# Kernel tuning notes

Measured on AMD Instinct MI355X. Metric: run time of the kernel, lower is better.

Reference implementation:

```python
import jax, jax.numpy as jnp
import numpy as np

N_NODES = 100000
NNZ = 3200000
D_FEAT = 128


def setup_inputs() -> dict:
    key = jax.random.key(0)
    k1, k2, k3 = jax.random.split(key, 3)
    indices = jax.random.randint(k1, (2, NNZ), 0, N_NODES, dtype=jnp.int64 if jax.config.jax_enable_x64 else jnp.int32)
    values = jax.random.normal(k2, (NNZ,), dtype=jnp.float32)
    b = jax.random.normal(k3, (N_NODES, D_FEAT), dtype=jnp.float32)
    return {"indices": indices, "values": values, "n_rows": N_NODES, "b": b}


def reference(indices, values, n_rows, b):
    # out = sparse_coo(indices, values, [n_rows, n_rows]) @ b
    # out[i] = sum_{e: row[e]==i} values[e] * b[col[e]]
    row, col = indices[0], indices[1]
    gathered = values[:, None] * b[col]              # [nnz, d]
    out = jax.ops.segment_sum(gathered, row, num_segments=n_rows)  # [n_rows, d]
    return out
```

## Files before the change

kernel.cpp:

```cpp
#include <hip/hip_runtime.h>


#define D_FEAT 128
#define RPB 256
#define BKT_SHIFT 8
#define MAX_NB 512
#define NBLK_SCAT 512
#define CHUNK_MAX 6400
#define STG_CAP 12288
#define RP_FLAG (1 << 30)

__device__ __forceinline__ unsigned short f2bf(float f) {
    unsigned u = __float_as_uint(f);
    u += 0x7FFFu + ((u >> 16) & 1u);
    return (unsigned short)(u >> 16);
}
__global__ void bconv_kernel(const float* __restrict__ bmat,
                             ushort* __restrict__ b16, int n4) {
    int i = blockIdx.x * blockDim.x + threadIdx.x;
    int gs = gridDim.x * blockDim.x;
    for (int k = i; k < n4; k += gs) {
        float4 v = reinterpret_cast<const float4*>(bmat)[k];
        ushort4 o;
        o.x = f2bf(v.x); o.y = f2bf(v.y); o.z = f2bf(v.z); o.w = f2bf(v.w);
        reinterpret_cast<ushort4*>(b16)[k] = o;
    }
}

__global__ void hist_kernel(const int* __restrict__ rowidx, int* __restrict__ hist,
                            int nnz) {
    __shared__ int lcnt[MAX_NB];
    for (int i = threadIdx.x; i < MAX_NB; i += blockDim.x) lcnt[i] = 0;
    __syncthreads();
    int gid = blockIdx.x * blockDim.x + threadIdx.x;
    int gsz = gridDim.x * blockDim.x;
    for (int e = gid; e < nnz; e += gsz)
        atomicAdd(&lcnt[rowidx[e] >> BKT_SHIFT], 1);
    __syncthreads();
    for (int i = threadIdx.x; i < MAX_NB; i += blockDim.x)
        if (lcnt[i]) atomicAdd(&hist[i], lcnt[i]);
}

__global__ void scan_kernel(const int* __restrict__ hist, int* __restrict__ gbase,
                            int* __restrict__ gcursor, int nb) {
    __shared__ int hs[512];
    int t = threadIdx.x;
    int v = hist[t];
    hs[t] = v;
    __syncthreads();
    for (int off = 1; off < 512; off <<= 1) {
        int u = (t >= off) ? hs[t - off] : 0;
        __syncthreads();
        hs[t] += u;
        __syncthreads();
    }
    int excl = hs[t] - v;
    if (t < nb) { gbase[t] = excl; gcursor[t] = excl; }
}

__global__ __launch_bounds__(512)
void scatter_kernel(const int* __restrict__ rowidx, const int* __restrict__ colidx,
                    const float* __restrict__ vals, int* __restrict__ gcursor,
                    float2* __restrict__ cv, int nnz, int nb) {
    __shared__ int loff[MAX_NB];
    __shared__ int cur[MAX_NB];
    __shared__ int gpos[MAX_NB];
    __shared__ ushort bktof[CHUNK_MAX];
    __shared__ float2 stage[CHUNK_MAX];
    int* scanbuf = (int*)stage;

    int t = threadIdx.x;
    int chunk = (nnz + gridDim.x - 1) / gridDim.x;
    int beg = blockIdx.x * chunk;
    int end = min(beg + chunk, nnz);
    int n = end - beg;

    for (int i = t; i < MAX_NB; i += 512) loff[i] = 0;
    __syncthreads();
    for (int e = beg + t; e < end; e += 512)
        atomicAdd(&loff[rowidx[e] >> BKT_SHIFT], 1);
    __syncthreads();

    int v = loff[t];
    scanbuf[t] = v;
    __syncthreads();
    for (int off = 1; off < 512; off <<= 1) {
        int u = (t >= off) ? scanbuf[t - off] : 0;
        __syncthreads();
        scanbuf[t] += u;
        __syncthreads();
    }
    int excl = scanbuf[t] - v;
    __syncthreads();
    loff[t] = excl;
    cur[t] = excl;
    __syncthreads();

    for (int e = beg + t; e < end; e += 512) {
        int r = rowidx[e];
        int bkt = r >> BKT_SHIFT;
        int pos = atomicAdd(&cur[bkt], 1);
        int pack = ((r & (RPB - 1)) << 17) | colidx[e];
        stage[pos] = make_float2(__int_as_float(pack), vals[e]);
        bktof[pos] = (ushort)bkt;
    }
    __syncthreads();

    if (t < nb) {
        int cnt = cur[t] - loff[t];
        if (cnt > 0) gpos[t] = atomicAdd(&gcursor[t], cnt);
    }
    __syncthreads();

    for (int i = t; i < n; i += 512) {
        int bkt = bktof[i];
        cv[gpos[bkt] + (i - loff[bkt])] = stage[i];
    }
}

__global__ __launch_bounds__(256)
void rowsort_kernel(const int* __restrict__ gbase, const int* __restrict__ gend,
                    float2* __restrict__ cv, int* __restrict__ rowptr,
                    int n_rows, int nb) {
    __shared__ float2 stg[STG_CAP];
    __shared__ int bin[RPB];
    __shared__ int sc[RPB];
    __shared__ int cur[RPB];
    int t = threadIdx.x;
    int bkt = blockIdx.x;
    int beg = gbase[bkt], end = gend[bkt];
    int n = end - beg;

    if (bkt == nb - 1 && t == 0) rowptr[n_rows] = end;

    if (n > STG_CAP) {
        int row = bkt * RPB + t;
        if (row < n_rows) rowptr[row] = beg | RP_FLAG;
        return;
    }

    bin[t] = 0;
    __syncthreads();
    for (int i = t; i < n; i += 256) {
        float2 p = cv[beg + i];
        stg[i] = p;
        atomicAdd(&bin[__float_as_int(p.x) >> 17], 1);
    }
    __syncthreads();
    int v = bin[t];
    sc[t] = v;
    __syncthreads();
    for (int off = 1; off < 256; off <<= 1) {
        int u = (t >= off) ? sc[t - off] : 0;
        __syncthreads();
        sc[t] += u;
        __syncthreads();
    }
    int excl = sc[t] - v;
    cur[t] = excl;
    int row = bkt * RPB + t;
    if (row < n_rows) rowptr[row] = beg + excl;
    __syncthreads();
    for (int i = t; i < n; i += 256) {
        float2 p = stg[i];
        int pos = atomicAdd(&cur[__float_as_int(p.x) >> 17], 1);
        cv[beg + pos] = p;
    }
}

__device__ __forceinline__ float bf2f(unsigned short h) {
    return __uint_as_float((unsigned)h << 16);
}
__global__ __launch_bounds__(256)
void rowmm16_kernel(const int* __restrict__ rowptr, const int* __restrict__ gbase,
                    const int* __restrict__ gend, const float2* __restrict__ cv,
                    const ushort* __restrict__ b16, float* __restrict__ out,
                    int n_rows) {
    int wid  = (blockIdx.x * blockDim.x + threadIdx.x) >> 6;
    int lane = threadIdx.x & 63;
    if (wid >= n_rows) return;

    const ushort2* bp = reinterpret_cast<const ushort2*>(b16) + lane;
    float2 acc = make_float2(0.f, 0.f);

    int rp = rowptr[wid];
    if (rp & RP_FLAG) {
        int bkt = wid >> BKT_SHIFT;
        int beg = gbase[bkt], end = gend[bkt];
        int myrl = wid & (RPB - 1);
        for (int j = beg; j < end; ++j) {
            float2 p = cv[j];
            int pack = __float_as_int(p.x);
            if ((pack >> 17) == myrl) {
                ushort2 u = bp[(size_t)(pack & 0x1FFFF) * (D_FEAT / 2)];
                acc.x += p.y * bf2f(u.x);  acc.y += p.y * bf2f(u.y);
            }
        }
    } else {
        int beg = rp;
        int end = rowptr[wid + 1] & ~RP_FLAG;
        int j = beg;
        for (; j + 7 < end; j += 8) {
            float2 p0 = cv[j],     p1 = cv[j + 1];
            float2 p2 = cv[j + 2], p3 = cv[j + 3];
            float2 p4 = cv[j + 4], p5 = cv[j + 5];
            float2 p6 = cv[j + 6], p7 = cv[j + 7];
            ushort2 u0 = bp[(size_t)(__float_as_int(p0.x) & 0x1FFFF) * (D_FEAT / 2)];
            ushort2 u1 = bp[(size_t)(__float_as_int(p1.x) & 0x1FFFF) * (D_FEAT / 2)];
            ushort2 u2 = bp[(size_t)(__float_as_int(p2.x) & 0x1FFFF) * (D_FEAT / 2)];
            ushort2 u3 = bp[(size_t)(__float_as_int(p3.x) & 0x1FFFF) * (D_FEAT / 2)];
            ushort2 u4 = bp[(size_t)(__float_as_int(p4.x) & 0x1FFFF) * (D_FEAT / 2)];
            ushort2 u5 = bp[(size_t)(__float_as_int(p5.x) & 0x1FFFF) * (D_FEAT / 2)];
            ushort2 u6 = bp[(size_t)(__float_as_int(p6.x) & 0x1FFFF) * (D_FEAT / 2)];
            ushort2 u7 = bp[(size_t)(__float_as_int(p7.x) & 0x1FFFF) * (D_FEAT / 2)];
            acc.x += p0.y * bf2f(u0.x);  acc.y += p0.y * bf2f(u0.y);
            acc.x += p1.y * bf2f(u1.x);  acc.y += p1.y * bf2f(u1.y);
            acc.x += p2.y * bf2f(u2.x);  acc.y += p2.y * bf2f(u2.y);
            acc.x += p3.y * bf2f(u3.x);  acc.y += p3.y * bf2f(u3.y);
            acc.x += p4.y * bf2f(u4.x);  acc.y += p4.y * bf2f(u4.y);
            acc.x += p5.y * bf2f(u5.x);  acc.y += p5.y * bf2f(u5.y);
            acc.x += p6.y * bf2f(u6.x);  acc.y += p6.y * bf2f(u6.y);
            acc.x += p7.y * bf2f(u7.x);  acc.y += p7.y * bf2f(u7.y);
        }
        for (; j < end; ++j) {
            float2 p = cv[j];
            ushort2 u = bp[(size_t)(__float_as_int(p.x) & 0x1FFFF) * (D_FEAT / 2)];
            acc.x += p.y * bf2f(u.x);  acc.y += p.y * bf2f(u.y);
        }
    }
    reinterpret_cast<float2*>(out + (size_t)wid * D_FEAT)[lane] = acc;
}

__global__ __launch_bounds__(256)
void rowmm_kernel(const int* __restrict__ rowptr, const int* __restrict__ gbase,
                  const int* __restrict__ gend, const float2* __restrict__ cv,
                  const float* __restrict__ bmat, float* __restrict__ out,
                  int n_rows) {
    int wid  = (blockIdx.x * blockDim.x + threadIdx.x) >> 6;
    int lane = threadIdx.x & 63;
    if (wid >= n_rows) return;
    const float2* bp = reinterpret_cast<const float2*>(bmat) + lane;
    float2 acc = make_float2(0.f, 0.f);
    int rp = rowptr[wid];
    if (rp & RP_FLAG) {
        int bkt = wid >> BKT_SHIFT;
        int beg = gbase[bkt], end = gend[bkt];
        int myrl = wid & (RPB - 1);
        for (int j = beg; j < end; ++j) {
            float2 p = cv[j];
            int pack = __float_as_int(p.x);
            if ((pack >> 17) == myrl) {
                float2 v = bp[(size_t)(pack & 0x1FFFF) * (D_FEAT / 2)];
                acc.x += p.y * v.x;  acc.y += p.y * v.y;
            }
        }
    } else {
        int beg = rp, end = rowptr[wid + 1] & ~RP_FLAG;
        for (int j = beg; j < end; ++j) {
            float2 p = cv[j];
            float2 v = bp[(size_t)(__float_as_int(p.x) & 0x1FFFF) * (D_FEAT / 2)];
            acc.x += p.y * v.x;  acc.y += p.y * v.y;
        }
    }
    reinterpret_cast<float2*>(out + (size_t)wid * D_FEAT)[lane] = acc;
}

extern "C" void kernel_launch(void* const* d_in, const int* in_sizes, int n_in,
                              void* d_out, int out_size, void* d_ws, size_t ws_size,
                              hipStream_t stream) {
    const int*   indices = (const int*)d_in[0];
    const float* values  = (const float*)d_in[1];
    const float* b       = (const float*)d_in[3];
    float*       out     = (float*)d_out;

    const int nnz    = in_sizes[1];
    const int n_rows = out_size / D_FEAT;
    const int nb     = (n_rows + RPB - 1) / RPB;
    const int* rowidx = indices;
    const int* colidx = indices + nnz;

    int*    hist    = (int*)d_ws;
    int*    gbase   = hist + MAX_NB;
    int*    gcursor = gbase + MAX_NB;
    int*    rowptr  = gcursor + MAX_NB;
    size_t  off     = (3 * MAX_NB + (size_t)n_rows + 1) * sizeof(int);
    off = (off + 15) & ~(size_t)15;

    size_t b16_bytes = (size_t)n_rows * D_FEAT * sizeof(ushort);
    size_t cv_bytes  = (size_t)nnz * sizeof(float2);
    bool   use16     = (off + b16_bytes + cv_bytes) <= ws_size;

    ushort* b16 = (ushort*)((char*)d_ws + off);
    float2* cv  = (float2*)((char*)d_ws + off + (use16 ? b16_bytes : 0));

    hipMemsetAsync(hist, 0, MAX_NB * sizeof(int), stream);
    if (use16)
        bconv_kernel<<<1024, 256, 0, stream>>>(b, b16, n_rows * D_FEAT / 4);
    hist_kernel<<<512, 256, 0, stream>>>(rowidx, hist, nnz);
    scan_kernel<<<1, 512, 0, stream>>>(hist, gbase, gcursor, nb);
    scatter_kernel<<<NBLK_SCAT, 512, 0, stream>>>(rowidx, colidx, values, gcursor, cv, nnz, nb);
    rowsort_kernel<<<nb, 256, 0, stream>>>(gbase, gcursor, cv, rowptr, n_rows, nb);
    if (use16)
        rowmm16_kernel<<<(n_rows * 64 + 255) / 256, 256, 0, stream>>>(rowptr, gbase, gcursor,
                                                                      cv, b16, out, n_rows);
    else
        rowmm_kernel<<<(n_rows * 64 + 255) / 256, 256, 0, stream>>>(rowptr, gbase, gcursor,
                                                                    cv, b, out, n_rows);
}
```

Measured before the change: 255.5 us.

## Halve row-bucket size and sort entries by column tile within each row

```diff
diff --git a/kernel.cpp b/kernel.cpp
--- a/kernel.cpp
+++ b/kernel.cpp
@@ -2,12 +2,14 @@
 
 
 #define D_FEAT 128
-#define RPB 256
-#define BKT_SHIFT 8
-#define MAX_NB 512
+#define RPB 128
+#define BKT_SHIFT 7
+#define MAX_NB 1024
 #define NBLK_SCAT 512
 #define CHUNK_MAX 6400
-#define STG_CAP 12288
+#define STG_CAP 6144
+#define CT_SHIFT 13
+#define NKEY (RPB * 16)
 #define RP_FLAG (1 << 30)
 
 __device__ __forceinline__ unsigned short f2bf(float f) {
@@ -45,8 +47,8 @@
                             int* __restrict__ gcursor, int nb) {
     __shared__ int hs[512];
     int t = threadIdx.x;
-    int v = hist[t];
-    hs[t] = v;
+    int v0 = hist[2 * t], v1 = hist[2 * t + 1];
+    hs[t] = v0 + v1;
     __syncthreads();
     for (int off = 1; off < 512; off <<= 1) {
         int u = (t >= off) ? hs[t - off] : 0;
@@ -54,8 +56,9 @@
         hs[t] += u;
         __syncthreads();
     }
-    int excl = hs[t] - v;
-    if (t < nb) { gbase[t] = excl; gcursor[t] = excl; }
+    int excl = hs[t] - (v0 + v1);
+    if (2 * t < nb)     { gbase[2 * t] = excl;          gcursor[2 * t] = excl; }
+    if (2 * t + 1 < nb) { gbase[2 * t + 1] = excl + v0; gcursor[2 * t + 1] = excl + v0; }
 }
 
 __global__ __launch_bounds__(512)
@@ -81,8 +84,8 @@
         atomicAdd(&loff[rowidx[e] >> BKT_SHIFT], 1);
     __syncthreads();
 
-    int v = loff[t];
-    scanbuf[t] = v;
+    int v0 = loff[2 * t], v1 = loff[2 * t + 1];
+    scanbuf[t] = v0 + v1;
     __syncthreads();
     for (int off = 1; off < 512; off <<= 1) {
         int u = (t >= off) ? scanbuf[t - off] : 0;
@@ -90,10 +93,10 @@
         scanbuf[t] += u;
         __syncthreads();
     }
-    int excl = scanbuf[t] - v;
-    __syncthreads();
-    loff[t] = excl;
-    cur[t] = excl;
+    int excl = scanbuf[t] - (v0 + v1);
+    __syncthreads();
+    loff[2 * t] = excl;       loff[2 * t + 1] = excl + v0;
+    cur[2 * t]  = excl;       cur[2 * t + 1]  = excl + v0;
     __syncthreads();
 
     for (int e = beg + t; e < end; e += 512) {
@@ -106,9 +109,9 @@
     }
     __syncthreads();
 
-    if (t < nb) {
-        int cnt = cur[t] - loff[t];
-        if (cnt > 0) gpos[t] = atomicAdd(&gcursor[t], cnt);
+    for (int i = t; i < nb; i += 512) {
+        int cnt = cur[i] - loff[i];
+        if (cnt > 0) gpos[i] = atomicAdd(&gcursor[i], cnt);
     }
     __syncthreads();
 
@@ -123,9 +126,9 @@
                     float2* __restrict__ cv, int* __restrict__ rowptr,
                     int n_rows, int nb) {
     __shared__ float2 stg[STG_CAP];
-    __shared__ int bin[RPB];
-    __shared__ int sc[RPB];
-    __shared__ int cur[RPB];
+    __shared__ int bin[NKEY];
+    __shared__ int cur[NKEY];
+    __shared__ int part[256];
     int t = threadIdx.x;
     int bkt = blockIdx.x;
     int beg = gbase[bkt], end = gend[bkt];
@@ -134,36 +137,53 @@
     if (bkt == nb - 1 && t == 0) rowptr[n_rows] = end;
 
     if (n > STG_CAP) {
-        int row = bkt * RPB + t;
-        if (row < n_rows) rowptr[row] = beg | RP_FLAG;
+        for (int rl = t; rl < RPB; rl += 256) {
+            int row = bkt * RPB + rl;
+            if (row < n_rows) rowptr[row] = beg | RP_FLAG;
+        }
         return;
     }
 
-    bin[t] = 0;
+    for (int i = t; i < NKEY; i += 256) bin[i] = 0;
     __syncthreads();
     for (int i = t; i < n; i += 256) {
         float2 p = cv[beg + i];
         stg[i] = p;
-        atomicAdd(&bin[__float_as_int(p.x) >> 17], 1);
-    }
-    __syncthreads();
-    int v = bin[t];
-    sc[t] = v;
+        int pk = __float_as_int(p.x);
+        int key = ((pk >> 17) << 4) | ((pk & 0x1FFFF) >> CT_SHIFT);
+        atomicAdd(&bin[key], 1);
+    }
+    __syncthreads();
+    int base8 = t * 8;
+    int loc[8];
+    int s = 0;
+    #pragma unroll
+    for (int k = 0; k < 8; ++k) { loc[k] = bin[base8 + k]; s += loc[k]; }
+    part[t] = s;
     __syncthreads();
     for (int off = 1; off < 256; off <<= 1) {
-        int u = (t >= off) ? sc[t - off] : 0;
-        __syncthreads();
-        sc[t] += u;
-        __syncthreads();
-    }
-    int excl = sc[t] - v;
-    cur[t] = excl;
-    int row = bkt * RPB + t;
-    if (row < n_rows) rowptr[row] = beg + excl;
+        int u = (t >= off) ? part[t - off] : 0;
+        __syncthreads();
+        part[t] += u;
+        __syncthreads();
+    }
+    int run = part[t] - s;
+    #pragma unroll
+    for (int k = 0; k < 8; ++k) {
+        int key = base8 + k;
+        cur[key] = run;
+        if ((key & 15) == 0) {
+            int row = bkt * RPB + (key >> 4);
+            if (row < n_rows) rowptr[row] = beg + run;
+        }
+        run += loc[k];
+    }
     __syncthreads();
     for (int i = t; i < n; i += 256) {
         float2 p = stg[i];
-        int pos = atomicAdd(&cur[__float_as_int(p.x) >> 17], 1);
+        int pk = __float_as_int(p.x);
+        int key = ((pk >> 17) << 4) | ((pk & 0x1FFFF) >> CT_SHIFT);
+        int pos = atomicAdd(&cur[key], 1);
         cv[beg + pos] = p;
     }
 }
```

New measurement: 251.9 us. About the same (-1.4%).
